# Performance work log

Measured on AMD Instinct MI355X. Metric: run time of the kernel, lower is better.

## Reference

```python
import jax, jax.numpy as jnp
import numpy as np

N = 10000   # num_nodes
F = 64      # latent_dim
U = 128     # num_units
B = 8       # batch
K = 2       # gcn_step
E = 160000  # edges (avg degree 16)
M = 2 * K + 1  # num_matrices = len(supports)*gcn_step + 1


def setup_inputs() -> dict:
    rng = np.random.default_rng(0)
    rows = rng.integers(0, N, E).astype(np.int32)
    cols = rng.integers(0, N, E).astype(np.int32)
    vals = (rng.random(E).astype(np.float32) + 0.1)
    # random-walk normalization D^{-1} A, per the original utils.calculate_random_walk_matrix
    deg_out = np.zeros(N, np.float32); np.add.at(deg_out, rows, vals)
    deg_in = np.zeros(N, np.float32); np.add.at(deg_in, cols, vals)
    # support1 = (D_out^{-1} A)^T : out[c] += vals/d_out[r] * x[r]  -> dst=cols, src=rows
    w1 = vals / np.maximum(deg_out[rows], 1e-8)
    # support2 = (D_in^{-1} A^T)^T : out[r] += vals/d_in[c] * x[c]  -> dst=rows, src=cols
    w2 = vals / np.maximum(deg_in[cols], 1e-8)

    key = jax.random.key(0)
    ks = jax.random.split(key, 4)

    def xavier(k, shape):
        std = (2.0 / (shape[0] + shape[1])) ** 0.5
        return jax.random.normal(k, shape, jnp.float32) * std

    return {
        'y': jax.random.normal(ks[0], (B, N * F), jnp.float32),
        'W_lat': xavier(ks[1], (M * F, F)),
        'b_lat': jnp.ones((F,), jnp.float32),   # bias_start=1.0, shared (keyed by length)
        'W_units': xavier(ks[2], (M * F, U)),
        'b_units': jnp.zeros((U,), jnp.float32),
        'W_final': xavier(ks[3], (M * U, F)),
        'sup1_w': jnp.asarray(w1),
        'sup2_w': jnp.asarray(w2),
        'edge_rows': jnp.asarray(rows),
        'edge_cols': jnp.asarray(cols),
    }


def _spmm(dst, src, w, x):
    # sparse matmul S @ x with S given as COO edge list; x: (N, Fin, B)
    return jax.ops.segment_sum(w[:, None, None] * x[src], dst, num_segments=N)


def _gconv(x, supports, W, b):
    # x: (B, N, Fin) -> (B, N*Fout); Chebyshev diffusion convolution
    Bsz, n, fin = x.shape
    x0 = jnp.transpose(x, (1, 2, 0))  # (N, Fin, B)
    xs = [x0]
    for dst, src, w in supports:
        xk_2 = x0
        x1 = _spmm(dst, src, w, x0)
        xs.append(x1)
        for _ in range(2, K + 1):
            x2 = 2.0 * _spmm(dst, src, w, x1) - xk_2
            xs.append(x2)
            xk_2, x1 = x1, x2
    X = jnp.stack(xs, axis=-1)                       # (N, Fin, B, M)
    X = jnp.transpose(X, (2, 0, 1, 3)).reshape(Bsz * n, fin * len(xs))  # feature-major, matrix-minor
    out = X @ W + b
    return out.reshape(Bsz, n * W.shape[1])


def reference(y, W_lat, b_lat, W_units, b_units, W_final, sup1_w, sup2_w, edge_rows, edge_cols):
    supports = [(edge_cols, edge_rows, sup1_w), (edge_rows, edge_cols, sup2_w)]
    x = y.reshape(B, N, F)
    # theta gate (bias_start=1.0 via shared b_lat)
    theta = jax.nn.sigmoid(_gconv(x, supports, W_lat, b_lat))
    # ode_func_net: gen_layers=1 hidden gconv + final gconv (final bias is shared b_lat!)
    c = jnp.tanh(_gconv(x, supports, W_units, b_units)).reshape(B, N, U)
    c = jnp.tanh(_gconv(c, supports, W_final, b_lat))
    return -theta * c
```

## Files before the change

### kernel.cpp

```cpp
#include <hip/hip_runtime.h>

#define N_NODES 10000
#define NEDGE 160000
#define NB 80000
#define SCAN_CH 40

typedef unsigned int u32;
typedef unsigned short u16;
typedef __attribute__((ext_vector_type(8))) short short8;
typedef __attribute__((ext_vector_type(4))) float float4v;

__device__ __forceinline__ float bf2f(u16 h) { return __uint_as_float(((u32)h) << 16); }
__device__ __forceinline__ u16 f2bf(float f) {
    u32 u = __float_as_uint(f);
    return (u16)((u + 0x7fffu + ((u >> 16) & 1u)) >> 16);
}
__device__ __forceinline__ float lo16(u32 u) { return __uint_as_float(u << 16); }
__device__ __forceinline__ float hi16(u32 u) { return __uint_as_float(u & 0xffff0000u); }
__device__ __forceinline__ u32 pack2(float a, float b) {
    return (u32)f2bf(a) | (((u32)f2bf(b)) << 16);
}
__device__ __forceinline__ float fast_tanh(float v) {
    return 1.f - 2.f / (__expf(2.f * v) + 1.f);
}

__global__ __launch_bounds__(256) void prep_kernel(
    const float2* __restrict__ y, u32* __restrict__ X0,
    const float* __restrict__ W_lat, const float* __restrict__ W_units,
    u16* __restrict__ bpk12,
    const float* __restrict__ W_final, u16* __restrict__ bpkP,
    int* __restrict__ cnt) {
    int b = blockIdx.x, t = threadIdx.x;
    if (b < 10000) {
        int idx = b * 256 + t;
        int fh = idx & 31;
        int rb = idx >> 5;
        int bb = rb & 7;
        int n = rb >> 3;
        float2 v = y[((size_t)bb * N_NODES + n) * 32 + fh];
        X0[idx] = pack2(v.x, v.y);
    } else if (b < 10240) {
        int idx = (b - 10000) * 256 + t;
        int j = idx & 7;
        int lane = (idx >> 3) & 63;
        int rest = idx >> 9;
        int ct = rest % 12;
        int ks = rest / 12;
        int k = ks * 32 + (lane >> 4) * 8 + j;
        int col = ct * 16 + (lane & 15);
        int wrow = (k % 64) * 5 + (k / 64);
        float v = (col < 64) ? W_lat[wrow * 64 + col] : W_units[wrow * 128 + (col - 64)];
        bpk12[idx] = f2bf(v);
    } else if (b < 10400) {
        int idx = (b - 10240) * 256 + t;
        int j8 = idx & 7;
        int lane = (idx >> 3) & 63;
        int rest = idx >> 9;
        int ct = rest % 20;
        int ks = rest / 20;
        int k = ks * 32 + (lane >> 4) * 8 + j8;
        int col = ct * 16 + (lane & 15);
        int slot = col >> 6, j = col & 63;
        float v;
        if (slot == 0)
            v = W_final[(k * 5 + 0) * 64 + j] - W_final[(k * 5 + 2) * 64 + j] -
                W_final[(k * 5 + 4) * 64 + j];
        else
            v = W_final[(k * 5 + slot) * 64 + j];
        bpkP[idx] = f2bf(v);
    } else {
        int idx = (b - 10400) * 256 + t;
        if (idx < 2 * N_NODES) cnt[idx] = 0;
    }
}

__global__ void count_kernel(const int* __restrict__ rows, const int* __restrict__ cols,
                             int* __restrict__ cnt1, int* __restrict__ cnt2) {
    int e = blockIdx.x * 256 + threadIdx.x;
    if (e < NEDGE) {
        atomicAdd(&cnt1[cols[e]], 1);
        atomicAdd(&cnt2[rows[e]], 1);
    }
}

__global__ void blocksum_kernel(const int* __restrict__ cnt, int* __restrict__ bsums) {
    __shared__ int red[4];
    int arr = blockIdx.x / SCAN_CH;
    int c = blockIdx.x % SCAN_CH;
    int idx = c * 256 + threadIdx.x;
    int v = (idx < N_NODES) ? cnt[arr * N_NODES + idx] : 0;
#pragma unroll
    for (int off = 32; off; off >>= 1) v += __shfl_down(v, off, 64);
    int wv = threadIdx.x >> 6, ln = threadIdx.x & 63;
    if (ln == 0) red[wv] = v;
    __syncthreads();
    if (threadIdx.x == 0) bsums[blockIdx.x] = red[0] + red[1] + red[2] + red[3];
}

__global__ void scanmid_kernel(int* __restrict__ bsums, int* __restrict__ rowptr1,
                               int* __restrict__ rowptr2) {
    __shared__ int lds[128];
    int t = threadIdx.x;
    int seg = t >> 6, pos = t & 63;
    int v = (pos < SCAN_CH) ? bsums[seg * SCAN_CH + pos] : 0;
    lds[t] = v;
    __syncthreads();
    for (int off = 1; off < 64; off <<= 1) {
        int add = (pos >= off) ? lds[t - off] : 0;
        __syncthreads();
        lds[t] += add;
        __syncthreads();
    }
    if (pos < SCAN_CH) bsums[seg * SCAN_CH + pos] = pos ? lds[t - 1] : 0;
    if (t == 0) { rowptr1[N_NODES] = NEDGE; rowptr2[N_NODES] = NEDGE; }
}

__global__ void scanapply_kernel(int* __restrict__ cnt, const int* __restrict__ bsums,
                                 int* __restrict__ rowptr1, int* __restrict__ rowptr2) {
    __shared__ int lds[256];
    int arr = blockIdx.x / SCAN_CH;
    int c = blockIdx.x % SCAN_CH;
    int idx = c * 256 + threadIdx.x;
    bool ok = idx < N_NODES;
    int v = ok ? cnt[arr * N_NODES + idx] : 0;
    int t = threadIdx.x;
    lds[t] = v;
    __syncthreads();
    for (int off = 1; off < 256; off <<= 1) {
        int add = (t >= off) ? lds[t - off] : 0;
        __syncthreads();
        lds[t] += add;
        __syncthreads();
    }
    int excl = lds[t] - v + bsums[blockIdx.x];
    if (ok) {
        int* rp = arr ? rowptr2 : rowptr1;
        rp[idx] = excl;
        cnt[arr * N_NODES + idx] = excl;
    }
}

__global__ void scatter_kernel(const int* __restrict__ rows, const int* __restrict__ cols,
                               const float* __restrict__ w1, const float* __restrict__ w2,
                               int* __restrict__ cur1, int* __restrict__ cur2,
                               int2* __restrict__ edges1, int2* __restrict__ edges2) {
    int e = blockIdx.x * 256 + threadIdx.x;
    if (e < NEDGE) {
        int r = rows[e], c = cols[e];
        int p1 = atomicAdd(&cur1[c], 1);
        edges1[p1] = make_int2(r, __float_as_int(w1[e]));
        int p2 = atomicAdd(&cur2[r], 1);
        edges2[p2] = make_int2(c, __float_as_int(w2[e]));
    }
}

__device__ __forceinline__ void gacc(float* acc, float w, uint4 u) {
    acc[0] += w * lo16(u.x); acc[1] += w * hi16(u.x);
    acc[2] += w * lo16(u.y); acc[3] += w * hi16(u.y);
    acc[4] += w * lo16(u.z); acc[5] += w * hi16(u.z);
    acc[6] += w * lo16(u.w); acc[7] += w * hi16(u.w);
}

__device__ __forceinline__ void gather_row(const u32* __restrict__ Xin,
                                           const int* __restrict__ rp,
                                           const int2* __restrict__ eg,
                                           int n, int lane, float* acc) {
    int e0 = rp[n], e1 = rp[n + 1];
    for (int base = e0; base < e1; base += 64) {
        int m = min(64, e1 - base);
        int2 me = make_int2(0, 0);
        if (lane < m) me = eg[base + lane];
        int j = 0;
        for (; j + 4 <= m; j += 4) {
            int s0 = __shfl(me.x, j, 64);
            int s1 = __shfl(me.x, j + 1, 64);
            int s2 = __shfl(me.x, j + 2, 64);
            int s3 = __shfl(me.x, j + 3, 64);
            float w0 = __int_as_float(__shfl(me.y, j, 64));
            float w1 = __int_as_float(__shfl(me.y, j + 1, 64));
            float w2 = __int_as_float(__shfl(me.y, j + 2, 64));
            float w3 = __int_as_float(__shfl(me.y, j + 3, 64));
            uint4 u0 = *(const uint4*)(Xin + (size_t)s0 * 256 + lane * 4);
            uint4 u1 = *(const uint4*)(Xin + (size_t)s1 * 256 + lane * 4);
            uint4 u2 = *(const uint4*)(Xin + (size_t)s2 * 256 + lane * 4);
            uint4 u3 = *(const uint4*)(Xin + (size_t)s3 * 256 + lane * 4);
            gacc(acc, w0, u0);
            gacc(acc, w1, u1);
            gacc(acc, w2, u2);
            gacc(acc, w3, u3);
        }
        for (; j < m; j++) {
            int src = __shfl(me.x, j, 64);
            float w = __int_as_float(__shfl(me.y, j, 64));
            uint4 u = *(const uint4*)(Xin + (size_t)src * 256 + lane * 4);
            gacc(acc, w, u);
        }
    }
}

__global__ __launch_bounds__(256) void spmm2_kernel(
    const u32* __restrict__ XinA, const u32* __restrict__ XprevA, u32* __restrict__ XoutA,
    const u32* __restrict__ XinB, const u32* __restrict__ XprevB, u32* __restrict__ XoutB,
    const int* __restrict__ rowptr1, const int2* __restrict__ edges1,
    const int* __restrict__ rowptr2, const int2* __restrict__ edges2,
    float alpha, float beta) {
    int lane = threadIdx.x & 63;
    int v = blockIdx.x * 4 + (threadIdx.x >> 6);
    if (v >= 2 * N_NODES) return;
    bool hB = v >= N_NODES;
    int n = hB ? v - N_NODES : v;
    const u32* Xin = hB ? XinB : XinA;
    const u32* Xprev = hB ? XprevB : XprevA;
    u32* Xout = hB ? XoutB : XoutA;
    const int* rp = hB ? rowptr2 : rowptr1;
    const int2* eg = hB ? edges2 : edges1;

    float acc[8] = {0.f, 0.f, 0.f, 0.f, 0.f, 0.f, 0.f, 0.f};
    gather_row(Xin, rp, eg, n, lane, acc);

    size_t o = (size_t)n * 256 + lane * 4;
    if (beta != 0.f) {
        uint4 p = *(const uint4*)(Xprev + o);
        acc[0] = alpha * acc[0] + beta * lo16(p.x); acc[1] = alpha * acc[1] + beta * hi16(p.x);
        acc[2] = alpha * acc[2] + beta * lo16(p.y); acc[3] = alpha * acc[3] + beta * hi16(p.y);
        acc[4] = alpha * acc[4] + beta * lo16(p.z); acc[5] = alpha * acc[5] + beta * hi16(p.z);
        acc[6] = alpha * acc[6] + beta * lo16(p.w); acc[7] = alpha * acc[7] + beta * hi16(p.w);
    } else {
#pragma unroll
        for (int i = 0; i < 8; i++) acc[i] *= alpha;
    }
    uint4 r;
    r.x = pack2(acc[0], acc[1]);
    r.y = pack2(acc[2], acc[3]);
    r.z = pack2(acc[4], acc[5]);
    r.w = pack2(acc[6], acc[7]);
    *(uint4*)(Xout + o) = r;
}

__global__ __launch_bounds__(256) void spmm_final_kernel(
    const u32* __restrict__ T1, const u32* __restrict__ T2,
    const u32* __restrict__ Q, const u32* __restrict__ theta,
    const int* __restrict__ rowptr1, const int2* __restrict__ edges1,
    const int* __restrict__ rowptr2, const int2* __restrict__ edges2,
    float* __restrict__ outF) {
    int lane = threadIdx.x & 63;
    int n = blockIdx.x * 4 + (threadIdx.x >> 6);
    if (n >= N_NODES) return;

    float acc[8] = {0.f, 0.f, 0.f, 0.f, 0.f, 0.f, 0.f, 0.f};
    gather_row(T1, rowptr1, edges1, n, lane, acc);
    gather_row(T2, rowptr2, edges2, n, lane, acc);

    size_t o = (size_t)n * 256 + lane * 4;
    uint4 q = *(const uint4*)(Q + o);
    uint4 th = *(const uint4*)(theta + o);
    float res[8];
    res[0] = -lo16(th.x) * fast_tanh(lo16(q.x) + acc[0]);
    res[1] = -hi16(th.x) * fast_tanh(hi16(q.x) + acc[1]);
    res[2] = -lo16(th.y) * fast_tanh(lo16(q.y) + acc[2]);
    res[3] = -hi16(th.y) * fast_tanh(hi16(q.y) + acc[3]);
    res[4] = -lo16(th.z) * fast_tanh(lo16(q.z) + acc[4]);
    res[5] = -hi16(th.z) * fast_tanh(hi16(q.z) + acc[5]);
    res[6] = -lo16(th.w) * fast_tanh(lo16(q.w) + acc[6]);
    res[7] = -hi16(th.w) * fast_tanh(hi16(q.w) + acc[7]);
    int b = lane >> 3;
    int f0 = ((lane * 4) & 31) * 2;
    float* dst = outF + (size_t)b * (N_NODES * 64) + (size_t)n * 64 + f0;
    *(float4*)(dst) = make_float4(res[0], res[1], res[2], res[3]);
    *(float4*)(dst + 4) = make_float4(res[4], res[5], res[6], res[7]);
}

struct Slabs { const u16* p[5]; };

template <int FIN, int NM, int NOUT, int NSPLIT, int MODE>
__global__ __launch_bounds__(256) void gemm_kernel(
    Slabs A, const u16* __restrict__ Bp, const float* __restrict__ bias1,
    const float* __restrict__ bias2, u16* __restrict__ O1, u16* __restrict__ O2) {
    constexpr int K = NM * FIN;
    constexpr int KS = K / 32;
    constexpr int CTT = NOUT / 16;
    constexpr int CT = CTT / NSPLIT;
    int lane = threadIdx.x & 63;
    int wave = threadIdx.x >> 6;
    int rowBase = (blockIdx.x / NSPLIT) * 64 + wave * 16;
    int ctBase = (blockIdx.x % NSPLIT) * CT;
    int mrow = lane & 15;
    int kq = lane >> 4;

    float4v acc[CT];
#pragma unroll
    for (int c = 0; c < CT; c++) acc[c] = (float4v){0.f, 0.f, 0.f, 0.f};

#pragma unroll
    for (int ks = 0; ks < KS; ks++) {
        int k = ks * 32 + kq * 8;
        int m = k / FIN;
        int koff = k % FIN;
        short8 a = *(const short8*)(A.p[m] + (size_t)(rowBase + mrow) * FIN + koff);
        short8 b[CT];
#pragma unroll
        for (int ct = 0; ct < CT; ct++)
            b[ct] = *(const short8*)(Bp + ((size_t)(ks * CTT + ctBase + ct) * 64 + lane) * 8);
#pragma unroll
        for (int ct = 0; ct < CT; ct++)
            acc[ct] = __builtin_amdgcn_mfma_f32_16x16x32_bf16(a, b[ct], acc[ct], 0, 0, 0);
    }

    int rowq = rowBase + kq * 4;
#pragma unroll
    for (int ct = 0; ct < CT; ct++) {
        int col = (ctBase + ct) * 16 + mrow;
        float bsv;
        if (MODE == 0) bsv = (col < 64) ? bias1[col] : 0.f;
        else bsv = (col < 64) ? bias1[col] : bias2[col - 64];
#pragma unroll
        for (int i = 0; i < 4; i++) {
            float v = acc[ct][i] + bsv;
            int r = rowq + i;
            if (MODE == 0) {
                O1[(size_t)(col >> 6) * ((size_t)NB * 64) + (size_t)r * 64 + (col & 63)] = f2bf(v);
            } else {
                if (col < 64) {
                    v = 1.f / (1.f + __expf(-v));
                    O1[(size_t)r * 64 + col] = f2bf(v);
                } else {
                    O2[(size_t)r * 128 + (col - 64)] = f2bf(fast_tanh(v));
                }
            }
        }
    }
}

extern "C" void kernel_launch(void* const* d_in, const int* in_sizes, int n_in,
                              void* d_out, int out_size, void* d_ws, size_t ws_size,
                              hipStream_t stream) {
    const float* y     = (const float*)d_in[0];
    const float* W_lat = (const float*)d_in[1];
    const float* b_lat = (const float*)d_in[2];
    const float* W_units = (const float*)d_in[3];
    const float* b_units = (const float*)d_in[4];
    const float* W_final = (const float*)d_in[5];
    const float* sup1w = (const float*)d_in[6];
    const float* sup2w = (const float*)d_in[7];
    const int* rows    = (const int*)d_in[8];
    const int* cols    = (const int*)d_in[9];
    float* out = (float*)d_out;

    char* ws = (char*)d_ws;
    size_t off = 0;
    auto alloc = [&](size_t bytes) -> void* {
        void* p = ws + off;
        off += (bytes + 511) & ~(size_t)511;
        return p;
    };
    int* rowptr1 = (int*)alloc((N_NODES + 1) * 4);
    int* rowptr2 = (int*)alloc((N_NODES + 1) * 4);
    int* cnt = (int*)alloc((size_t)2 * N_NODES * 4);
    int* cnt1 = cnt;
    int* cnt2 = cnt + N_NODES;
    int* bsums = (int*)alloc(2 * SCAN_CH * 4);
    int2* edges1 = (int2*)alloc((size_t)NEDGE * 8);
    int2* edges2 = (int2*)alloc((size_t)NEDGE * 8);
    u16* bpk12 = (u16*)alloc((size_t)61440 * 2);
    u16* bpkP = (u16*)alloc((size_t)40960 * 2);
    u16* theta = (u16*)alloc((size_t)NB * 64 * 2);
    u16* S = (u16*)alloc((size_t)5 * NB * 64 * 2);
    u16* H0 = (u16*)alloc((size_t)NB * 128 * 2);
    u16* T1 = (u16*)alloc((size_t)NB * 64 * 2);
    u16* T2 = (u16*)alloc((size_t)NB * 64 * 2);
    u16* P = S;

    const size_t SLAB = (size_t)NB * 64;

    prep_kernel<<<10479, 256, 0, stream>>>((const float2*)y, (u32*)S, W_lat, W_units,
                                           bpk12, W_final, bpkP, cnt);
    count_kernel<<<(NEDGE + 255) / 256, 256, 0, stream>>>(rows, cols, cnt1, cnt2);
    blocksum_kernel<<<2 * SCAN_CH, 256, 0, stream>>>(cnt, bsums);
    scanmid_kernel<<<1, 128, 0, stream>>>(bsums, rowptr1, rowptr2);
    scanapply_kernel<<<2 * SCAN_CH, 256, 0, stream>>>(cnt, bsums, rowptr1, rowptr2);
    scatter_kernel<<<(NEDGE + 255) / 256, 256, 0, stream>>>(rows, cols, sup1w, sup2w,
                                                            cnt1, cnt2, edges1, edges2);

    const u32* S0 = (const u32*)S;
    u32* X1 = (u32*)(S + 1 * SLAB);
    u32* X2 = (u32*)(S + 2 * SLAB);
    u32* X3 = (u32*)(S + 3 * SLAB);
    u32* X4 = (u32*)(S + 4 * SLAB);
    spmm2_kernel<<<5000, 256, 0, stream>>>(S0, nullptr, X1, S0, nullptr, X3,
                                           rowptr1, edges1, rowptr2, edges2, 1.f, 0.f);
    spmm2_kernel<<<5000, 256, 0, stream>>>(X1, S0, X2, X3, S0, X4,
                                           rowptr1, edges1, rowptr2, edges2, 2.f, -1.f);

    Slabs SX;
    for (int m = 0; m < 5; m++) SX.p[m] = S + (size_t)m * SLAB;
    gemm_kernel<64, 5, 192, 1, 1><<<1250, 256, 0, stream>>>(SX, bpk12, b_lat, b_units, theta, H0);

    Slabs SH;
    SH.p[0] = H0;
    gemm_kernel<128, 1, 320, 2, 0><<<2500, 256, 0, stream>>>(SH, bpkP, b_lat, nullptr, P, nullptr);

    const u32* Q  = (const u32*)(P + 0 * SLAB);
    const u32* P1 = (const u32*)(P + 1 * SLAB);
    const u32* P2 = (const u32*)(P + 2 * SLAB);
    const u32* P3 = (const u32*)(P + 3 * SLAB);
    const u32* P4 = (const u32*)(P + 4 * SLAB);
    spmm2_kernel<<<5000, 256, 0, stream>>>(P2, (const u32*)P1, (u32*)T1,
                                           P4, (const u32*)P3, (u32*)T2,
                                           rowptr1, edges1, rowptr2, edges2, 2.f, 1.f);
    spmm_final_kernel<<<2500, 256, 0, stream>>>((const u32*)T1, (const u32*)T2, Q,
                                                (const u32*)theta,
                                                rowptr1, edges1, rowptr2, edges2, out);
}
```

Measured before the change: 348.0 us.

## Split SpMM rows into column slices with two nodes per wave

Restructures the SpMM gather kernels so that each wave handles two nodes (one per half-wave), and each block covers only a 32-word column slice of the 256-word row. Grid size grows 4x. The intent is more parallelism and better latency hiding for the short rows (about 16 edges), since each half-wave now serves one node. The cost is that edge lists are reread once per column slice, 8x in total, and each load shrinks from 16 bytes to 4 bytes per lane. Loops are padded to multiples of 32 edges using zero weights.

```diff
diff --git a/kernel.cpp b/kernel.cpp
--- a/kernel.cpp
+++ b/kernel.cpp
@@ -154,120 +154,103 @@
     }
 }
 
-__device__ __forceinline__ void gacc(float* acc, float w, uint4 u) {
-    acc[0] += w * lo16(u.x); acc[1] += w * hi16(u.x);
-    acc[2] += w * lo16(u.y); acc[3] += w * hi16(u.y);
-    acc[4] += w * lo16(u.z); acc[5] += w * hi16(u.z);
-    acc[6] += w * lo16(u.w); acc[7] += w * hi16(u.w);
-}
-
-__device__ __forceinline__ void gather_row(const u32* __restrict__ Xin,
-                                           const int* __restrict__ rp,
-                                           const int2* __restrict__ eg,
-                                           int n, int lane, float* acc) {
+__device__ __forceinline__ void gather_slice(const u32* __restrict__ Xin,
+                                             const int* __restrict__ rp,
+                                             const int2* __restrict__ eg,
+                                             int n, int half, int hl, int coff,
+                                             float& a0, float& a1) {
     int e0 = rp[n], e1 = rp[n + 1];
-    for (int base = e0; base < e1; base += 64) {
-        int m = min(64, e1 - base);
+    int len = e1 - e0;
+    int olen = __shfl(len, (threadIdx.x & 63) ^ 32, 64);
+    int rounds = (max(len, olen) + 31) >> 5;
+    for (int r = 0; r < rounds; r++) {
         int2 me = make_int2(0, 0);
-        if (lane < m) me = eg[base + lane];
-        int j = 0;
-        for (; j + 4 <= m; j += 4) {
-            int s0 = __shfl(me.x, j, 64);
-            int s1 = __shfl(me.x, j + 1, 64);
-            int s2 = __shfl(me.x, j + 2, 64);
-            int s3 = __shfl(me.x, j + 3, 64);
-            float w0 = __int_as_float(__shfl(me.y, j, 64));
-            float w1 = __int_as_float(__shfl(me.y, j + 1, 64));
-            float w2 = __int_as_float(__shfl(me.y, j + 2, 64));
-            float w3 = __int_as_float(__shfl(me.y, j + 3, 64));
-            uint4 u0 = *(const uint4*)(Xin + (size_t)s0 * 256 + lane * 4);
-            uint4 u1 = *(const uint4*)(Xin + (size_t)s1 * 256 + lane * 4);
-            uint4 u2 = *(const uint4*)(Xin + (size_t)s2 * 256 + lane * 4);
-            uint4 u3 = *(const uint4*)(Xin + (size_t)s3 * 256 + lane * 4);
-            gacc(acc, w0, u0);
-            gacc(acc, w1, u1);
-            gacc(acc, w2, u2);
-            gacc(acc, w3, u3);
+        int ei = r * 32 + hl;
+        if (ei < len) me = eg[e0 + ei];
+        int sb = half << 5;
+#pragma unroll
+        for (int j = 0; j < 32; j += 4) {
+            int s0 = __shfl(me.x, sb + j, 64);
+            int s1 = __shfl(me.x, sb + j + 1, 64);
+            int s2 = __shfl(me.x, sb + j + 2, 64);
+            int s3 = __shfl(me.x, sb + j + 3, 64);
+            float w0 = __int_as_float(__shfl(me.y, sb + j, 64));
+            float w1 = __int_as_float(__shfl(me.y, sb + j + 1, 64));
+            float w2 = __int_as_float(__shfl(me.y, sb + j + 2, 64));
+            float w3 = __int_as_float(__shfl(me.y, sb + j + 3, 64));
+            u32 u0 = Xin[(size_t)s0 * 256 + coff + hl];
+            u32 u1 = Xin[(size_t)s1 * 256 + coff + hl];
+            u32 u2 = Xin[(size_t)s2 * 256 + coff + hl];
+            u32 u3 = Xin[(size_t)s3 * 256 + coff + hl];
+            a0 += w0 * lo16(u0); a1 += w0 * hi16(u0);
+            a0 += w1 * lo16(u1); a1 += w1 * hi16(u1);
+            a0 += w2 * lo16(u2); a1 += w2 * hi16(u2);
+            a0 += w3 * lo16(u3); a1 += w3 * hi16(u3);
         }
-        for (; j < m; j++) {
-            int src = __shfl(me.x, j, 64);
-            float w = __int_as_float(__shfl(me.y, j, 64));
-            uint4 u = *(const uint4*)(Xin + (size_t)src * 256 + lane * 4);
-            gacc(acc, w, u);
-        }
-    }
-}
-
-__global__ __launch_bounds__(256) void spmm2_kernel(
+    }
+}
+
+__global__ __launch_bounds__(256) void spmm8_kernel(
     const u32* __restrict__ XinA, const u32* __restrict__ XprevA, u32* __restrict__ XoutA,
     const u32* __restrict__ XinB, const u32* __restrict__ XprevB, u32* __restrict__ XoutB,
     const int* __restrict__ rowptr1, const int2* __restrict__ edges1,
     const int* __restrict__ rowptr2, const int2* __restrict__ edges2,
     float alpha, float beta) {
     int lane = threadIdx.x & 63;
-    int v = blockIdx.x * 4 + (threadIdx.x >> 6);
-    if (v >= 2 * N_NODES) return;
-    bool hB = v >= N_NODES;
-    int n = hB ? v - N_NODES : v;
+    int wave = threadIdx.x >> 6;
+    int half = lane >> 5, hl = lane & 31;
+    int col = blockIdx.x & 7;
+    int g = blockIdx.x >> 3;
+    int coff = col * 32;
+    bool hB = g >= 1250;
+    int n = (hB ? g - 1250 : g) * 8 + wave * 2 + half;
     const u32* Xin = hB ? XinB : XinA;
     const u32* Xprev = hB ? XprevB : XprevA;
     u32* Xout = hB ? XoutB : XoutA;
     const int* rp = hB ? rowptr2 : rowptr1;
     const int2* eg = hB ? edges2 : edges1;
 
-    float acc[8] = {0.f, 0.f, 0.f, 0.f, 0.f, 0.f, 0.f, 0.f};
-    gather_row(Xin, rp, eg, n, lane, acc);
-
-    size_t o = (size_t)n * 256 + lane * 4;
+    float a0 = 0.f, a1 = 0.f;
+    gather_slice(Xin, rp, eg, n, half, hl, coff, a0, a1);
+
+    size_t o = (size_t)n * 256 + coff + hl;
+    float r0 = alpha * a0, r1 = alpha * a1;
     if (beta != 0.f) {
-        uint4 p = *(const uint4*)(Xprev + o);
-        acc[0] = alpha * acc[0] + beta * lo16(p.x); acc[1] = alpha * acc[1] + beta * hi16(p.x);
-        acc[2] = alpha * acc[2] + beta * lo16(p.y); acc[3] = alpha * acc[3] + beta * hi16(p.y);
-        acc[4] = alpha * acc[4] + beta * lo16(p.z); acc[5] = alpha * acc[5] + beta * hi16(p.z);
-        acc[6] = alpha * acc[6] + beta * lo16(p.w); acc[7] = alpha * acc[7] + beta * hi16(p.w);
-    } else {
-#pragma unroll
-        for (int i = 0; i < 8; i++) acc[i] *= alpha;
-    }
-    uint4 r;
-    r.x = pack2(acc[0], acc[1]);
-    r.y = pack2(acc[2], acc[3]);
-    r.z = pack2(acc[4], acc[5]);
-    r.w = pack2(acc[6], acc[7]);
-    *(uint4*)(Xout + o) = r;
-}
-
-__global__ __launch_bounds__(256) void spmm_final_kernel(
+        u32 p = Xprev[o];
+        r0 += beta * lo16(p);
+        r1 += beta * hi16(p);
+    }
+    Xout[o] = pack2(r0, r1);
+}
+
+__global__ __launch_bounds__(256) void spmm8_final_kernel(
     const u32* __restrict__ T1, const u32* __restrict__ T2,
     const u32* __restrict__ Q, const u32* __restrict__ theta,
     const int* __restrict__ rowptr1, const int2* __restrict__ edges1,
     const int* __restrict__ rowptr2, const int2* __restrict__ edges2,
     float* __restrict__ outF) {
     int lane = threadIdx.x & 63;
-    int n = blockIdx.x * 4 + (threadIdx.x >> 6);
-    if (n >= N_NODES) return;
-
-    float acc[8] = {0.f, 0.f, 0.f, 0.f, 0.f, 0.f, 0.f, 0.f};
-    gather_row(T1, rowptr1, edges1, n, lane, acc);
-    gather_row(T2, rowptr2, edges2, n, lane, acc);
-
-    size_t o = (size_t)n * 256 + lane * 4;
-    uint4 q = *(const uint4*)(Q + o);
-    uint4 th = *(const uint4*)(theta + o);
-    float res[8];
-    res[0] = -lo16(th.x) * fast_tanh(lo16(q.x) + acc[0]);
-    res[1] = -hi16(th.x) * fast_tanh(hi16(q.x) + acc[1]);
-    res[2] = -lo16(th.y) * fast_tanh(lo16(q.y) + acc[2]);
-    res[3] = -hi16(th.y) * fast_tanh(hi16(q.y) + acc[3]);
-    res[4] = -lo16(th.z) * fast_tanh(lo16(q.z) + acc[4]);
-    res[5] = -hi16(th.z) * fast_tanh(hi16(q.z) + acc[5]);
-    res[6] = -lo16(th.w) * fast_tanh(lo16(q.w) + acc[6]);
-    res[7] = -hi16(th.w) * fast_tanh(hi16(q.w) + acc[7]);
-    int b = lane >> 3;
-    int f0 = ((lane * 4) & 31) * 2;
-    float* dst = outF + (size_t)b * (N_NODES * 64) + (size_t)n * 64 + f0;
-    *(float4*)(dst) = make_float4(res[0], res[1], res[2], res[3]);
-    *(float4*)(dst + 4) = make_float4(res[4], res[5], res[6], res[7]);
+    int wave = threadIdx.x >> 6;
+    int half = lane >> 5, hl = lane & 31;
+    int col = blockIdx.x & 7;
+    int g = blockIdx.x >> 3;
+    int coff = col * 32;
+    int n = g * 8 + wave * 2 + half;
+
+    float a0 = 0.f, a1 = 0.f;
+    gather_slice(T1, rowptr1, edges1, n, half, hl, coff, a0, a1);
+    gather_slice(T2, rowptr2, edges2, n, half, hl, coff, a0, a1);
+
+    size_t o = (size_t)n * 256 + coff + hl;
+    u32 q = Q[o];
+    u32 th = theta[o];
+    float v0 = fast_tanh(lo16(q) + a0);
+    float v1 = fast_tanh(hi16(q) + a1);
+    int idx = coff + hl;
+    int b = idx >> 5;
+    int f0 = (idx & 31) * 2;
+    *(float2*)(outF + (size_t)b * (N_NODES * 64) + (size_t)n * 64 + f0) =
+        make_float2(-lo16(th) * v0, -hi16(th) * v1);
 }
 
 struct Slabs { const u16* p[5]; };
@@ -386,10 +369,10 @@
     u32* X2 = (u32*)(S + 2 * SLAB);
     u32* X3 = (u32*)(S + 3 * SLAB);
     u32* X4 = (u32*)(S + 4 * SLAB);
-    spmm2_kernel<<<5000, 256, 0, stream>>>(S0, nullptr, X1, S0, nullptr, X3,
-                                           rowptr1, edges1, rowptr2, edges2, 1.f, 0.f);
-    spmm2_kernel<<<5000, 256, 0, stream>>>(X1, S0, X2, X3, S0, X4,
-                                           rowptr1, edges1, rowptr2, edges2, 2.f, -1.f);
+    spmm8_kernel<<<20000, 256, 0, stream>>>(S0, nullptr, X1, S0, nullptr, X3,
+                                            rowptr1, edges1, rowptr2, edges2, 1.f, 0.f);
+    spmm8_kernel<<<20000, 256, 0, stream>>>(X1, S0, X2, X3, S0, X4,
+                                            rowptr1, edges1, rowptr2, edges2, 2.f, -1.f);
 
     Slabs SX;
     for (int m = 0; m < 5; m++) SX.p[m] = S + (size_t)m * SLAB;
@@ -404,10 +387,10 @@
     const u32* P2 = (const u32*)(P + 2 * SLAB);
     const u32* P3 = (const u32*)(P + 3 * SLAB);
     const u32* P4 = (const u32*)(P + 4 * SLAB);
-    spmm2_kernel<<<5000, 256, 0, stream>>>(P2, (const u32*)P1, (u32*)T1,
-                                           P4, (const u32*)P3, (u32*)T2,
-                                           rowptr1, edges1, rowptr2, edges2, 2.f, 1.f);
-    spmm_final_kernel<<<2500, 256, 0, stream>>>((const u32*)T1, (const u32*)T2, Q,
-                                                (const u32*)theta,
-                                                rowptr1, edges1, rowptr2, edges2, out);
-}
+    spmm8_kernel<<<20000, 256, 0, stream>>>(P2, (const u32*)P1, (u32*)T1,
+                                            P4, (const u32*)P3, (u32*)T2,
+                                            rowptr1, edges1, rowptr2, edges2, 2.f, 1.f);
+    spmm8_final_kernel<<<10000, 256, 0, stream>>>((const u32*)T1, (const u32*)T2, Q,
+                                                  (const u32*)theta,
+                                                  rowptr1, edges1, rowptr2, edges2, out);
+}
```

Result: slower. 417.7 us (+20.0%).

## Fuse CSR build and prep into one persistent kernel with grid barriers

Applied to the files above, without the earlier changes.

Merges the prep, count, block-sum, scan and scatter kernels into a single persistent kernel of 1024 blocks, separated by atomic-counter grid barriers. The cnt array and the barrier counter are now zeroed with a memset instead of inside a kernel. The goal is to remove several launch gaps and tail effects from small kernels. In exchange it depends on all 1024 blocks being co-resident for the spin barriers, and the serial per-block prefix over bsums adds a little work.

```diff
diff --git a/kernel.cpp b/kernel.cpp
--- a/kernel.cpp
+++ b/kernel.cpp
@@ -3,14 +3,13 @@
 #define N_NODES 10000
 #define NEDGE 160000
 #define NB 80000
-#define SCAN_CH 40
+#define GRID1 1024
 
 typedef unsigned int u32;
 typedef unsigned short u16;
 typedef __attribute__((ext_vector_type(8))) short short8;
 typedef __attribute__((ext_vector_type(4))) float float4v;
 
-__device__ __forceinline__ float bf2f(u16 h) { return __uint_as_float(((u32)h) << 16); }
 __device__ __forceinline__ u16 f2bf(float f) {
     u32 u = __float_as_uint(f);
     return (u16)((u + 0x7fffu + ((u >> 16) & 1u)) >> 16);
@@ -24,133 +23,128 @@
     return 1.f - 2.f / (__expf(2.f * v) + 1.f);
 }
 
-__global__ __launch_bounds__(256) void prep_kernel(
+__device__ __forceinline__ void gbar(int* ctr, int target) {
+    __syncthreads();
+    if (threadIdx.x == 0) {
+        __threadfence();
+        __hip_atomic_fetch_add(ctr, 1, __ATOMIC_RELEASE, __HIP_MEMORY_SCOPE_AGENT);
+        while (__hip_atomic_load(ctr, __ATOMIC_ACQUIRE, __HIP_MEMORY_SCOPE_AGENT) < target)
+            __builtin_amdgcn_s_sleep(2);
+        __threadfence();
+    }
+    __syncthreads();
+}
+
+static const size_t SLAB = (size_t)NB * 64;
+
+__global__ __launch_bounds__(256, 4) void csr_kernel(
     const float2* __restrict__ y, u32* __restrict__ X0,
     const float* __restrict__ W_lat, const float* __restrict__ W_units,
-    u16* __restrict__ bpk12,
-    const float* __restrict__ W_final, u16* __restrict__ bpkP,
-    int* __restrict__ cnt) {
-    int b = blockIdx.x, t = threadIdx.x;
-    if (b < 10000) {
-        int idx = b * 256 + t;
-        int fh = idx & 31;
-        int rb = idx >> 5;
-        int bb = rb & 7;
-        int n = rb >> 3;
-        float2 v = y[((size_t)bb * N_NODES + n) * 32 + fh];
-        X0[idx] = pack2(v.x, v.y);
-    } else if (b < 10240) {
-        int idx = (b - 10000) * 256 + t;
-        int j = idx & 7;
-        int lane = (idx >> 3) & 63;
-        int rest = idx >> 9;
-        int ct = rest % 12;
-        int ks = rest / 12;
-        int k = ks * 32 + (lane >> 4) * 8 + j;
-        int col = ct * 16 + (lane & 15);
-        int wrow = (k % 64) * 5 + (k / 64);
-        float v = (col < 64) ? W_lat[wrow * 64 + col] : W_units[wrow * 128 + (col - 64)];
-        bpk12[idx] = f2bf(v);
-    } else if (b < 10400) {
-        int idx = (b - 10240) * 256 + t;
-        int j8 = idx & 7;
-        int lane = (idx >> 3) & 63;
-        int rest = idx >> 9;
-        int ct = rest % 20;
-        int ks = rest / 20;
-        int k = ks * 32 + (lane >> 4) * 8 + j8;
-        int col = ct * 16 + (lane & 15);
-        int slot = col >> 6, j = col & 63;
-        float v;
-        if (slot == 0)
-            v = W_final[(k * 5 + 0) * 64 + j] - W_final[(k * 5 + 2) * 64 + j] -
-                W_final[(k * 5 + 4) * 64 + j];
-        else
-            v = W_final[(k * 5 + slot) * 64 + j];
-        bpkP[idx] = f2bf(v);
-    } else {
-        int idx = (b - 10400) * 256 + t;
-        if (idx < 2 * N_NODES) cnt[idx] = 0;
-    }
-}
-
-__global__ void count_kernel(const int* __restrict__ rows, const int* __restrict__ cols,
-                             int* __restrict__ cnt1, int* __restrict__ cnt2) {
-    int e = blockIdx.x * 256 + threadIdx.x;
-    if (e < NEDGE) {
-        atomicAdd(&cnt1[cols[e]], 1);
-        atomicAdd(&cnt2[rows[e]], 1);
-    }
-}
-
-__global__ void blocksum_kernel(const int* __restrict__ cnt, int* __restrict__ bsums) {
-    __shared__ int red[4];
-    int arr = blockIdx.x / SCAN_CH;
-    int c = blockIdx.x % SCAN_CH;
-    int idx = c * 256 + threadIdx.x;
-    int v = (idx < N_NODES) ? cnt[arr * N_NODES + idx] : 0;
-#pragma unroll
-    for (int off = 32; off; off >>= 1) v += __shfl_down(v, off, 64);
-    int wv = threadIdx.x >> 6, ln = threadIdx.x & 63;
-    if (ln == 0) red[wv] = v;
-    __syncthreads();
-    if (threadIdx.x == 0) bsums[blockIdx.x] = red[0] + red[1] + red[2] + red[3];
-}
-
-__global__ void scanmid_kernel(int* __restrict__ bsums, int* __restrict__ rowptr1,
-                               int* __restrict__ rowptr2) {
-    __shared__ int lds[128];
+    u16* __restrict__ bpk12, const float* __restrict__ W_final, u16* __restrict__ bpkP,
+    const int* __restrict__ rows, const int* __restrict__ cols,
+    const float* __restrict__ sup1w, const float* __restrict__ sup2w,
+    int* __restrict__ cnt, int* __restrict__ bsums, int* __restrict__ barrier,
+    int* __restrict__ rowptr1, int* __restrict__ rowptr2,
+    int2* __restrict__ edges1, int2* __restrict__ edges2) {
+    __shared__ int sh[256];
     int t = threadIdx.x;
-    int seg = t >> 6, pos = t & 63;
-    int v = (pos < SCAN_CH) ? bsums[seg * SCAN_CH + pos] : 0;
-    lds[t] = v;
-    __syncthreads();
-    for (int off = 1; off < 64; off <<= 1) {
-        int add = (pos >= off) ? lds[t - off] : 0;
+
+    for (int wb = blockIdx.x; wb < 11025; wb += GRID1) {
+        if (wb < 10000) {
+            int idx = wb * 256 + t;
+            int fh = idx & 31;
+            int rb = idx >> 5;
+            int bb = rb & 7;
+            int n = rb >> 3;
+            float2 v = y[((size_t)bb * N_NODES + n) * 32 + fh];
+            X0[idx] = pack2(v.x, v.y);
+        } else if (wb < 10240) {
+            int idx = (wb - 10000) * 256 + t;
+            int j = idx & 7;
+            int lane = (idx >> 3) & 63;
+            int rest = idx >> 9;
+            int ct = rest % 12;
+            int ks = rest / 12;
+            int k = ks * 32 + (lane >> 4) * 8 + j;
+            int col = ct * 16 + (lane & 15);
+            int wrow = (k % 64) * 5 + (k / 64);
+            float v = (col < 64) ? W_lat[wrow * 64 + col] : W_units[wrow * 128 + (col - 64)];
+            bpk12[idx] = f2bf(v);
+        } else if (wb < 10400) {
+            int idx = (wb - 10240) * 256 + t;
+            int j8 = idx & 7;
+            int lane = (idx >> 3) & 63;
+            int rest = idx >> 9;
+            int ct = rest % 20;
+            int ks = rest / 20;
+            int k = ks * 32 + (lane >> 4) * 8 + j8;
+            int col = ct * 16 + (lane & 15);
+            int slot = col >> 6, j = col & 63;
+            float v;
+            if (slot == 0)
+                v = W_final[(k * 5 + 0) * 64 + j] - W_final[(k * 5 + 2) * 64 + j] -
+                    W_final[(k * 5 + 4) * 64 + j];
+            else
+                v = W_final[(k * 5 + slot) * 64 + j];
+            bpkP[idx] = f2bf(v);
+        } else {
+            int e = (wb - 10400) * 256 + t;
+            atomicAdd(&cnt[cols[e]], 1);
+            atomicAdd(&cnt[N_NODES + rows[e]], 1);
+        }
+    }
+    gbar(barrier, GRID1);
+
+    for (int wb = blockIdx.x; wb < 80; wb += GRID1) {
+        int arr = wb / 40, c = wb % 40;
+        int idx = c * 256 + t;
+        int v = (idx < N_NODES) ? cnt[arr * N_NODES + idx] : 0;
+#pragma unroll
+        for (int off = 32; off; off >>= 1) v += __shfl_down(v, off, 64);
+        int wv = t >> 6, ln = t & 63;
+        if (ln == 0) sh[wv] = v;
         __syncthreads();
-        lds[t] += add;
+        if (t == 0) bsums[wb] = sh[0] + sh[1] + sh[2] + sh[3];
         __syncthreads();
     }
-    if (pos < SCAN_CH) bsums[seg * SCAN_CH + pos] = pos ? lds[t - 1] : 0;
-    if (t == 0) { rowptr1[N_NODES] = NEDGE; rowptr2[N_NODES] = NEDGE; }
-}
-
-__global__ void scanapply_kernel(int* __restrict__ cnt, const int* __restrict__ bsums,
-                                 int* __restrict__ rowptr1, int* __restrict__ rowptr2) {
-    __shared__ int lds[256];
-    int arr = blockIdx.x / SCAN_CH;
-    int c = blockIdx.x % SCAN_CH;
-    int idx = c * 256 + threadIdx.x;
-    bool ok = idx < N_NODES;
-    int v = ok ? cnt[arr * N_NODES + idx] : 0;
-    int t = threadIdx.x;
-    lds[t] = v;
-    __syncthreads();
-    for (int off = 1; off < 256; off <<= 1) {
-        int add = (t >= off) ? lds[t - off] : 0;
+    gbar(barrier, 2 * GRID1);
+
+    for (int wb = blockIdx.x; wb < 80; wb += GRID1) {
+        int arr = wb / 40, c = wb % 40;
+        int base = 0;
+        for (int i = 0; i < c; i++) base += bsums[arr * 40 + i];
+        int idx = c * 256 + t;
+        bool ok = idx < N_NODES;
+        int v = ok ? cnt[arr * N_NODES + idx] : 0;
+        sh[t] = v;
         __syncthreads();
-        lds[t] += add;
+        for (int off = 1; off < 256; off <<= 1) {
+            int add = (t >= off) ? sh[t - off] : 0;
+            __syncthreads();
+            sh[t] += add;
+            __syncthreads();
+        }
+        int excl = sh[t] - v + base;
+        if (ok) {
+            int* rp = arr ? rowptr2 : rowptr1;
+            rp[idx] = excl;
+            cnt[arr * N_NODES + idx] = excl;
+        }
         __syncthreads();
     }
-    int excl = lds[t] - v + bsums[blockIdx.x];
-    if (ok) {
-        int* rp = arr ? rowptr2 : rowptr1;
-        rp[idx] = excl;
-        cnt[arr * N_NODES + idx] = excl;
-    }
-}
-
-__global__ void scatter_kernel(const int* __restrict__ rows, const int* __restrict__ cols,
-                               const float* __restrict__ w1, const float* __restrict__ w2,
-                               int* __restrict__ cur1, int* __restrict__ cur2,
-                               int2* __restrict__ edges1, int2* __restrict__ edges2) {
-    int e = blockIdx.x * 256 + threadIdx.x;
-    if (e < NEDGE) {
+    if (blockIdx.x == 0 && t == 0) {
+        rowptr1[N_NODES] = NEDGE;
+        rowptr2[N_NODES] = NEDGE;
+    }
+    gbar(barrier, 3 * GRID1);
+
+    for (int wb = blockIdx.x; wb < 625; wb += GRID1) {
+        int e = wb * 256 + t;
         int r = rows[e], c = cols[e];
-        int p1 = atomicAdd(&cur1[c], 1);
-        edges1[p1] = make_int2(r, __float_as_int(w1[e]));
-        int p2 = atomicAdd(&cur2[r], 1);
-        edges2[p2] = make_int2(c, __float_as_int(w2[e]));
+        int p1 = atomicAdd(&cnt[c], 1);
+        edges1[p1] = make_int2(r, __float_as_int(sup1w[e]));
+        int p2 = atomicAdd(&cnt[N_NODES + r], 1);
+        edges2[p2] = make_int2(c, __float_as_int(sup2w[e]));
     }
 }
 
@@ -318,7 +312,7 @@
             float v = acc[ct][i] + bsv;
             int r = rowq + i;
             if (MODE == 0) {
-                O1[(size_t)(col >> 6) * ((size_t)NB * 64) + (size_t)r * 64 + (col & 63)] = f2bf(v);
+                O1[(size_t)(col >> 6) * SLAB + (size_t)r * 64 + (col & 63)] = f2bf(v);
             } else {
                 if (col < 64) {
                     v = 1.f / (1.f + __expf(-v));
@@ -334,7 +328,7 @@
 extern "C" void kernel_launch(void* const* d_in, const int* in_sizes, int n_in,
                               void* d_out, int out_size, void* d_ws, size_t ws_size,
                               hipStream_t stream) {
-    const float* y     = (const float*)d_in[0];
+    const float2* y    = (const float2*)d_in[0];
     const float* W_lat = (const float*)d_in[1];
     const float* b_lat = (const float*)d_in[2];
     const float* W_units = (const float*)d_in[3];
@@ -356,9 +350,8 @@
     int* rowptr1 = (int*)alloc((N_NODES + 1) * 4);
     int* rowptr2 = (int*)alloc((N_NODES + 1) * 4);
     int* cnt = (int*)alloc((size_t)2 * N_NODES * 4);
-    int* cnt1 = cnt;
-    int* cnt2 = cnt + N_NODES;
-    int* bsums = (int*)alloc(2 * SCAN_CH * 4);
+    int* barrier = (int*)alloc(1024);
+    int* bsums = (int*)alloc(80 * 4);
     int2* edges1 = (int2*)alloc((size_t)NEDGE * 8);
     int2* edges2 = (int2*)alloc((size_t)NEDGE * 8);
     u16* bpk12 = (u16*)alloc((size_t)61440 * 2);
@@ -368,18 +361,12 @@
     u16* H0 = (u16*)alloc((size_t)NB * 128 * 2);
     u16* T1 = (u16*)alloc((size_t)NB * 64 * 2);
     u16* T2 = (u16*)alloc((size_t)NB * 64 * 2);
-    u16* P = S;
-
-    const size_t SLAB = (size_t)NB * 64;
-
-    prep_kernel<<<10479, 256, 0, stream>>>((const float2*)y, (u32*)S, W_lat, W_units,
-                                           bpk12, W_final, bpkP, cnt);
-    count_kernel<<<(NEDGE + 255) / 256, 256, 0, stream>>>(rows, cols, cnt1, cnt2);
-    blocksum_kernel<<<2 * SCAN_CH, 256, 0, stream>>>(cnt, bsums);
-    scanmid_kernel<<<1, 128, 0, stream>>>(bsums, rowptr1, rowptr2);
-    scanapply_kernel<<<2 * SCAN_CH, 256, 0, stream>>>(cnt, bsums, rowptr1, rowptr2);
-    scatter_kernel<<<(NEDGE + 255) / 256, 256, 0, stream>>>(rows, cols, sup1w, sup2w,
-                                                            cnt1, cnt2, edges1, edges2);
+
+    hipMemsetAsync(cnt, 0, 80384 + 1024, stream);
+
+    csr_kernel<<<GRID1, 256, 0, stream>>>(y, (u32*)S, W_lat, W_units, bpk12, W_final, bpkP,
+                                          rows, cols, sup1w, sup2w, cnt, bsums, barrier,
+                                          rowptr1, rowptr2, edges1, edges2);
 
     const u32* S0 = (const u32*)S;
     u32* X1 = (u32*)(S + 1 * SLAB);
@@ -397,15 +384,14 @@
 
     Slabs SH;
     SH.p[0] = H0;
-    gemm_kernel<128, 1, 320, 2, 0><<<2500, 256, 0, stream>>>(SH, bpkP, b_lat, nullptr, P, nullptr);
-
-    const u32* Q  = (const u32*)(P + 0 * SLAB);
-    const u32* P1 = (const u32*)(P + 1 * SLAB);
-    const u32* P2 = (const u32*)(P + 2 * SLAB);
-    const u32* P3 = (const u32*)(P + 3 * SLAB);
-    const u32* P4 = (const u32*)(P + 4 * SLAB);
-    spmm2_kernel<<<5000, 256, 0, stream>>>(P2, (const u32*)P1, (u32*)T1,
-                                           P4, (const u32*)P3, (u32*)T2,
+    gemm_kernel<128, 1, 320, 2, 0><<<2500, 256, 0, stream>>>(SH, bpkP, b_lat, nullptr, S, nullptr);
+
+    const u32* Q  = (const u32*)(S + 0 * SLAB);
+    const u32* P1 = (const u32*)(S + 1 * SLAB);
+    const u32* P2 = (const u32*)(S + 2 * SLAB);
+    const u32* P3 = (const u32*)(S + 3 * SLAB);
+    const u32* P4 = (const u32*)(S + 4 * SLAB);
+    spmm2_kernel<<<5000, 256, 0, stream>>>(P2, P1, (u32*)T1, P4, P3, (u32*)T2,
                                            rowptr1, edges1, rowptr2, edges2, 2.f, 1.f);
     spmm_final_kernel<<<2500, 256, 0, stream>>>((const u32*)T1, (const u32*)T2, Q,
                                                 (const u32*)theta,
```

Result: slower. 767.7 us (+120.6%).
